# Kernel optimization log

Hardware: AMD Instinct MI355X
Metric: run time of the kernel (lower is better)

Reference implementation:

```python
import jax, jax.numpy as jnp
import numpy as np

N = 50000       # nodes
E = 1600000     # edges (avg degree 32)
IN = 128        # node_in_dim
D = 64          # node_out_dim (= GRU hidden)
H = 1           # heads
ED = 3          # edge_in_dim
STEPS = 3       # num_step_message_passing
EPS = 1e-5      # BatchNorm eps
SLOPE = 0.2     # LeakyReLU negative slope (GAT default)


def setup_inputs() -> dict:
    key = jax.random.key(0)
    ks = jax.random.split(key, 16)
    s_in = 1.0 / np.sqrt(IN)
    s_d = 1.0 / np.sqrt(D)
    return {
        "x": jax.random.normal(ks[0], (N, IN), jnp.float32),
        "edge_attr": jax.random.normal(ks[1], (E, ED), jnp.float32),
        "mlp_w": jax.random.normal(ks[2], (IN, D), jnp.float32) * s_in,
        "mlp_b": jnp.zeros((D,), jnp.float32),
        "bn_g": jnp.ones((D,), jnp.float32),
        "bn_b": jnp.zeros((D,), jnp.float32),
        "conv_w": jax.random.normal(ks[3], (D, H * D), jnp.float32) * s_d,
        "att_dst": jax.random.normal(ks[4], (H, D), jnp.float32) * s_d,
        "att_src": jax.random.normal(ks[5], (H, D), jnp.float32) * s_d,
        "att_edge": jax.random.normal(ks[6], (H, ED), jnp.float32) * s_d,
        "w_ih": jax.random.normal(ks[7], (3 * D, H * D), jnp.float32) * s_d,
        "w_hh": jax.random.normal(ks[8], (3 * D, D), jnp.float32) * s_d,
        "b_ih": jnp.zeros((3 * D,), jnp.float32),
        "b_hh": jnp.zeros((3 * D,), jnp.float32),
        "lin_w": jax.random.normal(ks[9], (IN, D), jnp.float32) * s_in,
        "lin_b": jnp.zeros((D,), jnp.float32),
        "edge_index": jax.random.randint(ks[10], (2, E), 0, N, jnp.int64),
    }


def _egat_conv(out, edge_attr, src, dst, conv_w, att_dst, att_src, att_edge):
    # out: [N, D] -> xt: [N, H, D]
    xt = (out @ conv_w).reshape(N, H, D)
    # per-node attention halves (avoid gathering twice): [N, H]
    a_dst_n = jnp.einsum("nhd,hd->nh", xt, att_dst)
    a_src_n = jnp.einsum("nhd,hd->nh", xt, att_src)
    # per-edge logits: [E, H]
    logits = a_dst_n[dst] + a_src_n[src] + edge_attr @ att_edge.T
    logits = jnp.where(logits >= 0, logits, SLOPE * logits)
    # segment softmax over destination nodes
    seg_max = jax.ops.segment_max(logits, dst, num_segments=N)  # [N, H]
    seg_max = jnp.where(jnp.isfinite(seg_max), seg_max, 0.0)
    expd = jnp.exp(logits - seg_max[dst])
    denom = jax.ops.segment_sum(expd, dst, num_segments=N)      # [N, H]
    alpha = expd / denom[dst]                                   # [E, H]
    # attention-weighted aggregation of source features
    msgs = alpha[:, :, None] * xt[src]                          # [E, H, D]
    agg = jax.ops.segment_sum(msgs, dst, num_segments=N)        # [N, H, D]
    return agg.reshape(N, H * D)


def _gru_cell(x_in, h, w_ih, w_hh, b_ih, b_hh):
    gi = x_in @ w_ih.T + b_ih
    gh = h @ w_hh.T + b_hh
    gi_r, gi_z, gi_n = jnp.split(gi, 3, axis=-1)
    gh_r, gh_z, gh_n = jnp.split(gh, 3, axis=-1)
    r = jax.nn.sigmoid(gi_r + gh_r)
    z = jax.nn.sigmoid(gi_z + gh_z)
    n = jnp.tanh(gi_n + r * gh_n)
    return (1.0 - z) * n + z * h


def reference(x, edge_attr, mlp_w, mlp_b, bn_g, bn_b, conv_w, att_dst,
              att_src, att_edge, w_ih, w_hh, b_ih, b_hh, lin_w, lin_b,
              edge_index):
    src, dst = edge_index[0], edge_index[1]
    # initial embedding: ReLU(BatchNorm(Linear(x))) with batch stats
    h0 = x @ mlp_w + mlp_b
    mu = jnp.mean(h0, axis=0)
    var = jnp.var(h0, axis=0)
    out = jax.nn.relu((h0 - mu) * jax.lax.rsqrt(var + EPS) * bn_g + bn_b)
    h = out
    for _ in range(STEPS):
        m = jax.nn.relu(_egat_conv(out, edge_attr, src, dst,
                                   conv_w, att_dst, att_src, att_edge))
        h = _gru_cell(m, h, w_ih, w_hh, b_ih, b_hh)
        out = h
    return x @ lin_w + lin_b + out
```

## Files before the change

kernel.cpp:

```cpp
#include <hip/hip_runtime.h>

typedef unsigned short ushort_t;
typedef unsigned int uint_t;
typedef __attribute__((ext_vector_type(8))) short bf16x8;
typedef __attribute__((ext_vector_type(4))) float f32x4;

#define N_NODES 50000
#define N_EDGES 1600000
#define NB_BKT 391
#define CAP_BKT 4608
#define CAP_B 6144
#define GBK 782
#define WPAD 72
#define APAD 64

__device__ __forceinline__ float bfu(ushort_t u) {
    return __uint_as_float(((uint_t)u) << 16);
}
__device__ __forceinline__ ushort_t f2b(float f) {
    uint_t x = __float_as_uint(f);
    uint_t r = (x + 0x7FFFu + ((x >> 16) & 1u)) >> 16;
    return (ushort_t)r;
}
__device__ __forceinline__ float sigm(float x) {
    return 1.0f / (1.0f + __expf(-x));
}
__device__ __forceinline__ float tanh_f(float x) {
    return 1.0f - 2.0f / (__expf(2.0f * x) + 1.0f);
}
__device__ __forceinline__ bf16x8 pack8(const float* v) {
    bf16x8 r;
#pragma unroll
    for (int j = 0; j < 8; ++j) r[j] = (short)f2b(v[j]);
    return r;
}
__device__ __forceinline__ int ld_src(const int* __restrict__ ei, int i, int f64) {
    return f64 ? ei[2 * i] : ei[i];
}
__device__ __forceinline__ int ld_dst(const int* __restrict__ ei, int i, int f64) {
    return f64 ? ei[2 * N_EDGES + 2 * i] : ei[N_EDGES + i];
}
__device__ __forceinline__ bool is_f64(const int* flag) { return flag[0] > 2048; }

__global__ void k_sentinel(float* __restrict__ out, int n) {
    int i = blockIdx.x * 256 + threadIdx.x;
    if (i < n) out[i] = 100.0f;
}

__global__ void k_prep(const float* __restrict__ w_ih, const float* __restrict__ w_hh,
                       const float* __restrict__ conv_w, const float* __restrict__ mlp_w,
                       const float* __restrict__ lin_w, const int* __restrict__ ei,
                       ushort_t* __restrict__ wb, ushort_t* __restrict__ cwb,
                       ushort_t* __restrict__ mlpT, ushort_t* __restrict__ linT,
                       int* __restrict__ flag, int* __restrict__ gtail) {
    int blk = blockIdx.x;
    if (blk < 176) {
        int t = blk * 256 + threadIdx.x;
        if (t < 24576) {
            const float* w = (t < 12288) ? w_ih : w_hh;
            wb[t] = f2b(w[t < 12288 ? t : t - 12288]);
        } else if (t < 28672) {
            int r = t - 24576;
            int j = r >> 6, k = r & 63;
            cwb[j * 64 + k] = f2b(conv_w[k * 64 + j]);
        } else if (t < 36864) {
            int r = t - 28672;
            int j = r >> 7, k = r & 127;
            mlpT[j * 128 + k] = f2b(mlp_w[k * 64 + j]);
        } else if (t < 45056) {
            int r = t - 36864;
            int j = r >> 7, k = r & 127;
            linT[j * 128 + k] = f2b(lin_w[k * 64 + j]);
        }
    } else if (blk == 176) {
        __shared__ int red[256];
        int tid = threadIdx.x;
        int zeros = 0;
#pragma unroll
        for (int j = 0; j < 16; ++j) {
            int slot = (tid * 16 + j) * 2 + 1;
            if (ei[slot] == 0) zeros++;
        }
        red[tid] = zeros;
        __syncthreads();
        for (int off = 128; off; off >>= 1) {
            if (tid < off) red[tid] += red[tid + off];
            __syncthreads();
        }
        if (tid == 0) flag[0] = red[0];
    } else {
        int b = (blk - 177) * 256 + threadIdx.x;
        if (b < NB_BKT) gtail[b * APAD] = b * CAP_BKT;
    }
}

__global__ __launch_bounds__(256) void k_embbkt(
    const int* __restrict__ ei, const int* __restrict__ flag,
    const float* __restrict__ ea, const float* __restrict__ ae,
    int* __restrict__ gtail, uint2* __restrict__ bkt, int e,
    const float* __restrict__ x, const ushort_t* __restrict__ mlpT,
    const float* __restrict__ mlp_b, float* __restrict__ h0, int n) {
    if (blockIdx.x < GBK) {
        __shared__ int cnt[NB_BKT];
        __shared__ int gbase[NB_BKT];
        for (int i = threadIdx.x; i < NB_BKT; i += 256) cnt[i] = 0;
        __syncthreads();
        int base = blockIdx.x * 2048;
        int f64 = is_f64(flag);
        float a0 = ae[0], a1 = ae[1], a2 = ae[2];
        uint_t w0[8], w1[8];
        int bk[8], rk[8];
#pragma unroll
        for (int j = 0; j < 8; ++j) {
            int i = base + j * 256 + threadIdx.x;
            bk[j] = -1;
            if (i < e) {
                int d = ld_dst(ei, i, f64);
                if ((uint_t)d < (uint_t)N_NODES) {
                    int s = ld_src(ei, i, f64);
                    if ((uint_t)s >= (uint_t)N_NODES) s = 0;
                    float ed = ea[i * 3] * a0 + ea[i * 3 + 1] * a1 + ea[i * 3 + 2] * a2;
                    bk[j] = d >> 7;
                    w0[j] = (uint_t)s | ((uint_t)(d & 127) << 16);
                    w1[j] = __float_as_uint(ed);
                    rk[j] = atomicAdd(&cnt[bk[j]], 1);
                }
            }
        }
        __syncthreads();
        for (int t = threadIdx.x; t < NB_BKT; t += 256) {
            int c = cnt[t];
            gbase[t] = c ? atomicAdd(&gtail[t * APAD], c) : 0;
        }
        __syncthreads();
#pragma unroll
        for (int j = 0; j < 8; ++j) {
            if (bk[j] >= 0) {
                int pos = gbase[bk[j]] + rk[j];
                if (pos < (bk[j] + 1) * CAP_BKT) {
                    uint2 p;
                    p.x = w0[j];
                    p.y = w1[j];
                    bkt[pos] = p;
                }
            }
        }
    } else {
        int lane = threadIdx.x & 63;
        int wv = threadIdx.x >> 6;
        int tile = (blockIdx.x - GBK) * 4 + wv;
        if (tile * 16 >= n) return;
        int nb16 = tile * 16;
        int mrow = lane & 15, q = lane >> 4;
        const float* xp = x + (nb16 + mrow) * 128 + q * 8;
        bf16x8 a[4];
#pragma unroll
        for (int kc = 0; kc < 4; ++kc) {
            float hv[8];
            const float* p = xp + kc * 32;
#pragma unroll
            for (int j = 0; j < 8; ++j) hv[j] = p[j];
            a[kc] = pack8(hv);
        }
        f32x4 acc[4];
#pragma unroll
        for (int t = 0; t < 4; ++t) acc[t] = (f32x4){0.f, 0.f, 0.f, 0.f};
#pragma unroll
        for (int kc = 0; kc < 4; ++kc) {
#pragma unroll
            for (int t = 0; t < 4; ++t) {
                bf16x8 b =
                    *(const bf16x8*)(mlpT + (t * 16 + mrow) * 128 + kc * 32 + q * 8);
                acc[t] = __builtin_amdgcn_mfma_f32_16x16x32_bf16(a[kc], b, acc[t], 0, 0, 0);
            }
        }
#pragma unroll
        for (int t = 0; t < 4; ++t) {
            int j = t * 16 + mrow;
            float bias = mlp_b[j];
#pragma unroll
            for (int r = 0; r < 4; ++r)
                h0[(nb16 + q * 4 + r) * 64 + j] = acc[t][r] + bias;
        }
    }
}

__global__ __launch_bounds__(256) void k_statsort(
    const int* __restrict__ gtail, const uint2* __restrict__ bkt,
    uint_t* __restrict__ pk, int* __restrict__ rs, int n,
    const float* __restrict__ h0, float* __restrict__ stats) {
    __shared__ char smem[26624];
    int tid = threadIdx.x;
    if (blockIdx.x < NB_BKT) {
        int* red = (int*)smem;
        int* cnt = (int*)(smem + 1024);
        int* sc = (int*)(smem + 1536);
        uint_t* stg = (uint_t*)(smem + 2048);
        int b = blockIdx.x;
        int partial = 0;
        for (int i = tid; i < b; i += 256)
            partial += min(gtail[i * APAD] - i * CAP_BKT, CAP_BKT);
        red[tid] = partial;
        __syncthreads();
        for (int off = 128; off; off >>= 1) {
            if (tid < off) red[tid] += red[tid + off];
            __syncthreads();
        }
        int obase = red[0];
        int node0 = b * 128;
        int nloc = min(128, n - node0);
        int size = min(gtail[b * APAD] - b * CAP_BKT, CAP_BKT);
        const uint2* bin = bkt + b * CAP_BKT;
        for (int i = tid; i < 128; i += 256) cnt[i] = 0;
        __syncthreads();
        for (int ofs = tid; ofs < size; ofs += 256) {
            int dlow = (bin[ofs].x >> 16) & 127;
            atomicAdd(&cnt[dlow], 1);
        }
        __syncthreads();
        if (tid < 128) sc[tid] = cnt[tid];
        __syncthreads();
        for (int off = 1; off < 128; off <<= 1) {
            int add = (tid < 128 && tid >= off) ? sc[tid - off] : 0;
            __syncthreads();
            if (tid < 128) sc[tid] += add;
            __syncthreads();
        }
        if (tid < 128) sc[tid] -= cnt[tid];
        __syncthreads();
        if (tid < nloc) rs[node0 + tid] = obase + sc[tid];
        if (b == NB_BKT - 1 && tid == 0) rs[n] = obase + size;
        for (int i = tid; i < 128; i += 256) cnt[i] = 0;
        __syncthreads();
        for (int ofs = tid; ofs < size; ofs += 256) {
            uint2 p = bin[ofs];
            int dlow = (p.x >> 16) & 127;
            int r = atomicAdd(&cnt[dlow], 1);
            int pos = sc[dlow] + r;
            uint_t q = (p.x & 0xFFFFu) | ((uint_t)f2b(__uint_as_float(p.y)) << 16);
            if (pos < CAP_B) stg[pos] = q;
            else pk[obase + pos] = q;
        }
        __syncthreads();
        int wlim = min(size, CAP_B);
        for (int ofs = tid; ofs < wlim; ofs += 256) pk[obase + ofs] = stg[ofs];
    } else {
        float* ssum = (float*)smem;
        float* ssq = (float*)(smem + 1024);
        int gid = (blockIdx.x - NB_BKT) * 256 + tid;
        int col = gid & 63;
        int rg = gid >> 6;
        float s = 0.f, s2 = 0.f;
        for (int row = rg; row < n; row += 1024) {
            float v = h0[row * 64 + col];
            s += v;
            s2 += v * v;
        }
        ssum[tid] = s;
        ssq[tid] = s2;
        __syncthreads();
        if (tid < 64) {
            s = ssum[tid] + ssum[tid + 64] + ssum[tid + 128] + ssum[tid + 192];
            s2 = ssq[tid] + ssq[tid + 64] + ssq[tid + 128] + ssq[tid + 192];
            atomicAdd(&stats[tid * APAD], s);
            atomicAdd(&stats[(64 + tid) * APAD], s2);
        }
    }
}

__global__ __launch_bounds__(256) void k_xt(float* __restrict__ h,
                                            const ushort_t* __restrict__ cwb,
                                            const float* __restrict__ att_dst,
                                            const float* __restrict__ att_src,
                                            const float* __restrict__ bn_g,
                                            const float* __restrict__ bn_b,
                                            const float* __restrict__ stats,
                                            float inv_n,
                                            ushort_t* __restrict__ xt,
                                            float* __restrict__ adst,
                                            float* __restrict__ asrc, int n) {
    __shared__ float scb[64], shb[64];
    {
        int tid = threadIdx.x;
        if (tid < 64) {
            float mu = stats[tid * APAD] * inv_n;
            float var = fmaxf(stats[(64 + tid) * APAD] * inv_n - mu * mu, 0.f);
            float sc = rsqrtf(var + 1e-5f) * bn_g[tid];
            scb[tid] = sc;
            shb[tid] = bn_b[tid] - mu * sc;
        }
        __syncthreads();
    }
    int lane = threadIdx.x & 63;
    int wv = threadIdx.x >> 6;
    int tile = blockIdx.x * 4 + wv;
    if (tile * 16 >= n) return;
    int nb16 = tile * 16;
    int mrow = lane & 15, q = lane >> 4;
    bf16x8 ah[2];
    {
        float* hp = h + (nb16 + mrow) * 64 + q * 8;
        float hv[8];
#pragma unroll
        for (int kh = 0; kh < 2; ++kh) {
            float* p = hp + kh * 32;
            int cb = kh * 32 + q * 8;
#pragma unroll
            for (int j = 0; j < 8; ++j) {
                hv[j] = fmaxf(p[j] * scb[cb + j] + shb[cb + j], 0.f);
                p[j] = hv[j];
            }
            ah[kh] = pack8(hv);
        }
    }
    f32x4 acc[4];
#pragma unroll
    for (int t = 0; t < 4; ++t) acc[t] = (f32x4){0.f, 0.f, 0.f, 0.f};
#pragma unroll
    for (int kh = 0; kh < 2; ++kh) {
#pragma unroll
        for (int t = 0; t < 4; ++t) {
            bf16x8 b = *(const bf16x8*)(cwb + (t * 16 + mrow) * 64 + kh * 32 + q * 8);
            acc[t] = __builtin_amdgcn_mfma_f32_16x16x32_bf16(ah[kh], b, acc[t], 0, 0, 0);
        }
    }
    float sd[4] = {0, 0, 0, 0}, ss[4] = {0, 0, 0, 0};
#pragma unroll
    for (int t = 0; t < 4; ++t) {
        int j = t * 16 + mrow;
        float ad = att_dst[j], as = att_src[j];
#pragma unroll
        for (int r = 0; r < 4; ++r) {
            float v = acc[t][r];
            xt[(nb16 + q * 4 + r) * 64 + j] = f2b(v);
            sd[r] += v * ad;
            ss[r] += v * as;
        }
    }
#pragma unroll
    for (int off = 1; off < 16; off <<= 1) {
#pragma unroll
        for (int r = 0; r < 4; ++r) {
            sd[r] += __shfl_xor(sd[r], off);
            ss[r] += __shfl_xor(ss[r], off);
        }
    }
    if (mrow == 0) {
#pragma unroll
        for (int r = 0; r < 4; ++r) {
            adst[nb16 + q * 4 + r] = sd[r];
            asrc[nb16 + q * 4 + r] = ss[r];
        }
    }
}

__global__ __launch_bounds__(256) void k_agg(const int* __restrict__ rs,
                                             const uint_t* __restrict__ pk,
                                             const float* __restrict__ adst,
                                             const float* __restrict__ asrc,
                                             const ushort_t* __restrict__ xt,
                                             ushort_t* __restrict__ m, int n) {
    __shared__ float s_w[4][64];
    __shared__ int s_s[4][64];
    int lane = threadIdx.x & 63;
    int wv = threadIdx.x >> 6;
    int v = blockIdx.x * 4 + wv;
    if (v >= n) return;
    int start = rs[v], end = rs[v + 1];
    if (start >= end) {
        m[v * 64 + lane] = 0;
        return;
    }
    float adv = adst[v];
    int g = lane >> 3;
    int cb = (lane & 7) * 8;
    float acc[8] = {0, 0, 0, 0, 0, 0, 0, 0};
    float dsum = 0.f;
    for (int base = start; base < end; base += 64) {
        int e = base + lane;
        float w = 0.f;
        int s = 0;
        if (e < end) {
            uint_t p = pk[e];
            s = (int)(p & 0xFFFFu);
            float l = adv + asrc[s] + bfu((ushort_t)(p >> 16));
            l = (l >= 0.f) ? l : 0.2f * l;
            w = __expf(l);
        }
        dsum += w;
        s_w[wv][lane] = w;
        s_s[wv][lane] = s;
        int cnt = min(64, end - base);
        int nb8 = (cnt + 7) >> 3;
        for (int tb = 0; tb < nb8; ++tb) {
            int sl = tb * 8 + g;
            float w8 = s_w[wv][sl];
            int s8 = s_s[wv][sl];
            uint4 qv = *(const uint4*)(xt + s8 * 64 + cb);
            acc[0] += w8 * __uint_as_float(qv.x << 16);
            acc[1] += w8 * __uint_as_float(qv.x & 0xFFFF0000u);
            acc[2] += w8 * __uint_as_float(qv.y << 16);
            acc[3] += w8 * __uint_as_float(qv.y & 0xFFFF0000u);
            acc[4] += w8 * __uint_as_float(qv.z << 16);
            acc[5] += w8 * __uint_as_float(qv.z & 0xFFFF0000u);
            acc[6] += w8 * __uint_as_float(qv.w << 16);
            acc[7] += w8 * __uint_as_float(qv.w & 0xFFFF0000u);
        }
    }
#pragma unroll
    for (int off = 32; off; off >>= 1) dsum += __shfl_xor(dsum, off);
#pragma unroll
    for (int off = 8; off < 64; off <<= 1) {
#pragma unroll
        for (int j = 0; j < 8; ++j) acc[j] += __shfl_xor(acc[j], off);
    }
    float inv = 1.0f / fmaxf(dsum, 1e-20f);
    if (g == 0) {
        uint4 o;
        o.x = (uint_t)f2b(fmaxf(acc[0] * inv, 0.f)) |
              ((uint_t)f2b(fmaxf(acc[1] * inv, 0.f)) << 16);
        o.y = (uint_t)f2b(fmaxf(acc[2] * inv, 0.f)) |
              ((uint_t)f2b(fmaxf(acc[3] * inv, 0.f)) << 16);
        o.z = (uint_t)f2b(fmaxf(acc[4] * inv, 0.f)) |
              ((uint_t)f2b(fmaxf(acc[5] * inv, 0.f)) << 16);
        o.w = (uint_t)f2b(fmaxf(acc[6] * inv, 0.f)) |
              ((uint_t)f2b(fmaxf(acc[7] * inv, 0.f)) << 16);
        *(uint4*)(m + v * 64 + cb) = o;
    }
}

__global__ __launch_bounds__(256) void k_gruxt(
    const ushort_t* __restrict__ mb, float* __restrict__ h,
    const ushort_t* __restrict__ wb, const ushort_t* __restrict__ cwb,
    const float* __restrict__ b_ih, const float* __restrict__ b_hh,
    const float* __restrict__ att_dst, const float* __restrict__ att_src,
    int do_xt, ushort_t* __restrict__ xt, float* __restrict__ adst,
    float* __restrict__ asrc, int n) {
    __shared__ ushort_t swb[384 * WPAD];
    __shared__ ushort_t scw[64 * WPAD];
    {
        const uint2* src = (const uint2*)wb;
        for (int g = threadIdx.x; g < 6144; g += 256) {
            uint2 v = src[g];
            int row = g >> 4;
            int col = (g & 15) * 4;
            *(uint2*)(swb + row * WPAD + col) = v;
        }
        const uint2* srcc = (const uint2*)cwb;
        for (int g = threadIdx.x; g < 1024; g += 256) {
            uint2 v = srcc[g];
            int row = g >> 4;
            int col = (g & 15) * 4;
            *(uint2*)(scw + row * WPAD + col) = v;
        }
    }
    __syncthreads();
    int lane = threadIdx.x & 63;
    int wv = threadIdx.x >> 6;
    int tile = blockIdx.x * 4 + wv;
    if (tile * 16 >= n) return;
    int nb16 = tile * 16;
    int mrow = lane & 15, q = lane >> 4;
    float hp[4][4];
#pragma unroll
    for (int t = 0; t < 4; ++t)
#pragma unroll
        for (int r = 0; r < 4; ++r)
            hp[t][r] = h[(nb16 + q * 4 + r) * 64 + t * 16 + mrow];
    bf16x8 am[2], ah[2];
    {
        const ushort_t* mp = mb + (nb16 + mrow) * 64 + q * 8;
        am[0] = *(const bf16x8*)(mp);
        am[1] = *(const bf16x8*)(mp + 32);
        const float* hpt = h + (nb16 + mrow) * 64 + q * 8;
        float hv[8];
#pragma unroll
        for (int j = 0; j < 8; ++j) hv[j] = hpt[j];
        ah[0] = pack8(hv);
#pragma unroll
        for (int j = 0; j < 8; ++j) hv[j] = hpt[32 + j];
        ah[1] = pack8(hv);
    }
    f32x4 acc[24];
#pragma unroll
    for (int t = 0; t < 24; ++t) acc[t] = (f32x4){0.f, 0.f, 0.f, 0.f};
#pragma unroll
    for (int kh = 0; kh < 2; ++kh) {
#pragma unroll
        for (int t = 0; t < 12; ++t) {
            bf16x8 b = *(const bf16x8*)(swb + (t * 16 + mrow) * WPAD + kh * 32 + q * 8);
            acc[t] = __builtin_amdgcn_mfma_f32_16x16x32_bf16(am[kh], b, acc[t], 0, 0, 0);
        }
#pragma unroll
        for (int t = 0; t < 12; ++t) {
            bf16x8 b =
                *(const bf16x8*)(swb + (192 + t * 16 + mrow) * WPAD + kh * 32 + q * 8);
            acc[12 + t] =
                __builtin_amdgcn_mfma_f32_16x16x32_bf16(ah[kh], b, acc[12 + t], 0, 0, 0);
        }
    }
#pragma unroll
    for (int t = 0; t < 4; ++t) {
        int j = t * 16 + mrow;
        float bir = b_ih[j], biz = b_ih[64 + j], bin = b_ih[128 + j];
        float bhr = b_hh[j], bhz = b_hh[64 + j], bhn = b_hh[128 + j];
#pragma unroll
        for (int r = 0; r < 4; ++r) {
            int node = nb16 + q * 4 + r;
            float gr = acc[t][r] + bir + acc[12 + t][r] + bhr;
            float gz = acc[4 + t][r] + biz + acc[16 + t][r] + bhz;
            float rr = sigm(gr);
            float zz = sigm(gz);
            float tt = acc[8 + t][r] + bin + rr * (acc[20 + t][r] + bhn);
            h[node * 64 + j] = (1.f - zz) * tanh_f(tt) + zz * hp[t][r];
        }
    }
    if (!do_xt) return;
    __threadfence_block();
    bf16x8 ah2[2];
    {
        const float* hpt = h + (nb16 + mrow) * 64 + q * 8;
        float hv[8];
#pragma unroll
        for (int j = 0; j < 8; ++j) hv[j] = hpt[j];
        ah2[0] = pack8(hv);
#pragma unroll
        for (int j = 0; j < 8; ++j) hv[j] = hpt[32 + j];
        ah2[1] = pack8(hv);
    }
    f32x4 xacc[4];
#pragma unroll
    for (int t = 0; t < 4; ++t) xacc[t] = (f32x4){0.f, 0.f, 0.f, 0.f};
#pragma unroll
    for (int kh = 0; kh < 2; ++kh) {
#pragma unroll
        for (int t = 0; t < 4; ++t) {
            bf16x8 b = *(const bf16x8*)(scw + (t * 16 + mrow) * WPAD + kh * 32 + q * 8);
            xacc[t] = __builtin_amdgcn_mfma_f32_16x16x32_bf16(ah2[kh], b, xacc[t], 0, 0, 0);
        }
    }
    float sd[4] = {0, 0, 0, 0}, ss[4] = {0, 0, 0, 0};
#pragma unroll
    for (int t = 0; t < 4; ++t) {
        int j = t * 16 + mrow;
        float ad = att_dst[j], as = att_src[j];
#pragma unroll
        for (int r = 0; r < 4; ++r) {
            float v = xacc[t][r];
            xt[(nb16 + q * 4 + r) * 64 + j] = f2b(v);
            sd[r] += v * ad;
            ss[r] += v * as;
        }
    }
#pragma unroll
    for (int off = 1; off < 16; off <<= 1) {
#pragma unroll
        for (int r = 0; r < 4; ++r) {
            sd[r] += __shfl_xor(sd[r], off);
            ss[r] += __shfl_xor(ss[r], off);
        }
    }
    if (mrow == 0) {
#pragma unroll
        for (int r = 0; r < 4; ++r) {
            adst[nb16 + q * 4 + r] = sd[r];
            asrc[nb16 + q * 4 + r] = ss[r];
        }
    }
}

__global__ __launch_bounds__(256) void k_out(const float* __restrict__ x,
                                             const ushort_t* __restrict__ linT,
                                             const float* __restrict__ lin_b,
                                             const float* __restrict__ h,
                                             float* __restrict__ out, int n) {
    int lane = threadIdx.x & 63;
    int wv = threadIdx.x >> 6;
    int tile = blockIdx.x * 4 + wv;
    if (tile * 16 >= n) return;
    int nb16 = tile * 16;
    int mrow = lane & 15, q = lane >> 4;
    const float* xp = x + (nb16 + mrow) * 128 + q * 8;
    bf16x8 a[4];
#pragma unroll
    for (int kc = 0; kc < 4; ++kc) {
        float hv[8];
        const float* p = xp + kc * 32;
#pragma unroll
        for (int j = 0; j < 8; ++j) hv[j] = p[j];
        a[kc] = pack8(hv);
    }
    f32x4 acc[4];
#pragma unroll
    for (int t = 0; t < 4; ++t) acc[t] = (f32x4){0.f, 0.f, 0.f, 0.f};
#pragma unroll
    for (int kc = 0; kc < 4; ++kc) {
#pragma unroll
        for (int t = 0; t < 4; ++t) {
            bf16x8 b = *(const bf16x8*)(linT + (t * 16 + mrow) * 128 + kc * 32 + q * 8);
            acc[t] = __builtin_amdgcn_mfma_f32_16x16x32_bf16(a[kc], b, acc[t], 0, 0, 0);
        }
    }
#pragma unroll
    for (int t = 0; t < 4; ++t) {
        int j = t * 16 + mrow;
        float bias = lin_b[j];
#pragma unroll
        for (int r = 0; r < 4; ++r) {
            int node = nb16 + q * 4 + r;
            out[node * 64 + j] = acc[t][r] + bias + h[node * 64 + j];
        }
    }
}

extern "C" void kernel_launch(void* const* d_in, const int* in_sizes, int n_in,
                              void* d_out, int out_size, void* d_ws, size_t ws_size,
                              hipStream_t stream) {
    const float* x = (const float*)d_in[0];
    const float* edge_attr = (const float*)d_in[1];
    const float* mlp_w = (const float*)d_in[2];
    const float* mlp_b = (const float*)d_in[3];
    const float* bn_g = (const float*)d_in[4];
    const float* bn_b = (const float*)d_in[5];
    const float* conv_w = (const float*)d_in[6];
    const float* att_dst = (const float*)d_in[7];
    const float* att_src = (const float*)d_in[8];
    const float* att_edge = (const float*)d_in[9];
    const float* w_ih = (const float*)d_in[10];
    const float* w_hh = (const float*)d_in[11];
    const float* b_ih = (const float*)d_in[12];
    const float* b_hh = (const float*)d_in[13];
    const float* lin_w = (const float*)d_in[14];
    const float* lin_b = (const float*)d_in[15];
    const int* ei = (const int*)d_in[16];

    char* ws = (char*)d_ws;
    float* f_h = (float*)(ws + 0);
    ushort_t* mb = (ushort_t*)(ws + 12800000);
    ushort_t* xt = (ushort_t*)(ws + 19200000);
    uint2* bkt = (uint2*)(ws + 25600000);
    uint_t* pk = (uint_t*)(ws + 40013824);
    float* f_adst = (float*)(ws + 46413824);
    float* f_asrc = (float*)(ws + 46614016);
    int* row_start = (int*)(ws + 46814208);
    float* stats = (float*)(ws + 47014656);
    int* flag = (int*)(ws + 47047424);
    ushort_t* wb = (ushort_t*)(ws + 47047936);
    ushort_t* cwb = (ushort_t*)(ws + 47097088);
    ushort_t* mlpT = (ushort_t*)(ws + 47105280);
    ushort_t* linT = (ushort_t*)(ws + 47121664);
    int* gtail = (int*)(ws + 47138048);

    const size_t needed = 47238144;
    if (ws_size < needed) {
        k_sentinel<<<(out_size + 255) / 256, 256, 0, stream>>>((float*)d_out, out_size);
        return;
    }

    const int n = N_NODES, e = N_EDGES;
    const int gT = ((n + 15) / 16 + 3) / 4;
    const int gN4 = (n + 3) / 4;
    const int gPrep = 176 + 1 + (NB_BKT + 255) / 256;
    const float inv_n = 1.0f / (float)n;

    hipMemsetAsync(stats, 0, 32768, stream);

    k_prep<<<gPrep, 256, 0, stream>>>(w_ih, w_hh, conv_w, mlp_w, lin_w, ei, wb, cwb,
                                      mlpT, linT, flag, gtail);
    k_embbkt<<<GBK + gT, 256, 0, stream>>>(ei, flag, edge_attr, att_edge, gtail, bkt, e,
                                           x, mlpT, mlp_b, f_h, n);
    k_statsort<<<NB_BKT + 256, 256, 0, stream>>>(gtail, bkt, pk, row_start, n, f_h,
                                                 stats);
    k_xt<<<gT, 256, 0, stream>>>(f_h, cwb, att_dst, att_src, bn_g, bn_b, stats, inv_n,
                                 xt, f_adst, f_asrc, n);

    for (int s = 0; s < 3; ++s) {
        k_agg<<<gN4, 256, 0, stream>>>(row_start, pk, f_adst, f_asrc, xt, mb, n);
        k_gruxt<<<gT, 256, 0, stream>>>(mb, f_h, wb, cwb, b_ih, b_hh, att_dst, att_src,
                                        (s < 2) ? 1 : 0, xt, f_adst, f_asrc, n);
    }

    k_out<<<gT, 256, 0, stream>>>(x, linT, lin_b, f_h, (float*)d_out, n);
}
```

Before: 368.8 us.

## Compute source attention logits from gathered features in aggregation; enlarge bucketing blocks

The aggregation kernel stops doing a separate random gather of the per-node source attention scalar. Instead it computes the source logit by dotting the already-gathered bf16 xt row with att_src, reduced across 8 lanes with shuffles, and then applies LeakyReLU and exp per edge inside the inner loop. This removes one scattered load per edge but adds extra FMAs, shuffles and exps per 8-edge group, and the logit now comes from bf16 xt rather than the fp32 asrc. Separately, the edge-bucketing kernel now processes 4096 edges per block with half as many blocks, so fewer global atomics are issued on the bucket tails.

```diff
diff --git a/kernel.cpp b/kernel.cpp
--- a/kernel.cpp
+++ b/kernel.cpp
@@ -10,7 +10,7 @@
 #define NB_BKT 391
 #define CAP_BKT 4608
 #define CAP_B 6144
-#define GBK 782
+#define GBK 391
 #define WPAD 72
 #define APAD 64
 
@@ -105,13 +105,13 @@
         __shared__ int gbase[NB_BKT];
         for (int i = threadIdx.x; i < NB_BKT; i += 256) cnt[i] = 0;
         __syncthreads();
-        int base = blockIdx.x * 2048;
+        int base = blockIdx.x * 4096;
         int f64 = is_f64(flag);
         float a0 = ae[0], a1 = ae[1], a2 = ae[2];
-        uint_t w0[8], w1[8];
-        int bk[8], rk[8];
-#pragma unroll
-        for (int j = 0; j < 8; ++j) {
+        uint_t w0[16], w1[16];
+        int bk[16], rk[16];
+#pragma unroll
+        for (int j = 0; j < 16; ++j) {
             int i = base + j * 256 + threadIdx.x;
             bk[j] = -1;
             if (i < e) {
@@ -134,7 +134,7 @@
         }
         __syncthreads();
 #pragma unroll
-        for (int j = 0; j < 8; ++j) {
+        for (int j = 0; j < 16; ++j) {
             if (bk[j] >= 0) {
                 int pos = gbase[bk[j]] + rk[j];
                 if (pos < (bk[j] + 1) * CAP_BKT) {
@@ -357,7 +357,7 @@
 __global__ __launch_bounds__(256) void k_agg(const int* __restrict__ rs,
                                              const uint_t* __restrict__ pk,
                                              const float* __restrict__ adst,
-                                             const float* __restrict__ asrc,
+                                             const float* __restrict__ att_src,
                                              const ushort_t* __restrict__ xt,
                                              ushort_t* __restrict__ m, int n) {
     __shared__ float s_w[4][64];
@@ -374,41 +374,59 @@
     float adv = adst[v];
     int g = lane >> 3;
     int cb = (lane & 7) * 8;
+    float asv[8];
+#pragma unroll
+    for (int j = 0; j < 8; ++j) asv[j] = att_src[cb + j];
     float acc[8] = {0, 0, 0, 0, 0, 0, 0, 0};
     float dsum = 0.f;
     for (int base = start; base < end; base += 64) {
         int e = base + lane;
-        float w = 0.f;
+        float et = 0.f;
         int s = 0;
         if (e < end) {
             uint_t p = pk[e];
             s = (int)(p & 0xFFFFu);
-            float l = adv + asrc[s] + bfu((ushort_t)(p >> 16));
-            l = (l >= 0.f) ? l : 0.2f * l;
-            w = __expf(l);
-        }
-        dsum += w;
-        s_w[wv][lane] = w;
+            et = bfu((ushort_t)(p >> 16));
+        }
+        s_w[wv][lane] = et;
         s_s[wv][lane] = s;
         int cnt = min(64, end - base);
         int nb8 = (cnt + 7) >> 3;
         for (int tb = 0; tb < nb8; ++tb) {
             int sl = tb * 8 + g;
-            float w8 = s_w[wv][sl];
+            float et8 = s_w[wv][sl];
             int s8 = s_s[wv][sl];
             uint4 qv = *(const uint4*)(xt + s8 * 64 + cb);
-            acc[0] += w8 * __uint_as_float(qv.x << 16);
-            acc[1] += w8 * __uint_as_float(qv.x & 0xFFFF0000u);
-            acc[2] += w8 * __uint_as_float(qv.y << 16);
-            acc[3] += w8 * __uint_as_float(qv.y & 0xFFFF0000u);
-            acc[4] += w8 * __uint_as_float(qv.z << 16);
-            acc[5] += w8 * __uint_as_float(qv.z & 0xFFFF0000u);
-            acc[6] += w8 * __uint_as_float(qv.w << 16);
-            acc[7] += w8 * __uint_as_float(qv.w & 0xFFFF0000u);
-        }
-    }
-#pragma unroll
-    for (int off = 32; off; off >>= 1) dsum += __shfl_xor(dsum, off);
+            float f0 = __uint_as_float(qv.x << 16);
+            float f1 = __uint_as_float(qv.x & 0xFFFF0000u);
+            float f2 = __uint_as_float(qv.y << 16);
+            float f3 = __uint_as_float(qv.y & 0xFFFF0000u);
+            float f4 = __uint_as_float(qv.z << 16);
+            float f5 = __uint_as_float(qv.z & 0xFFFF0000u);
+            float f6 = __uint_as_float(qv.w << 16);
+            float f7 = __uint_as_float(qv.w & 0xFFFF0000u);
+            float part = f0 * asv[0] + f1 * asv[1] + f2 * asv[2] + f3 * asv[3] +
+                         f4 * asv[4] + f5 * asv[5] + f6 * asv[6] + f7 * asv[7];
+            part += __shfl_xor(part, 1);
+            part += __shfl_xor(part, 2);
+            part += __shfl_xor(part, 4);
+            float l = adv + part + et8;
+            l = (l >= 0.f) ? l : 0.2f * l;
+            float w8 = (sl < cnt) ? __expf(l) : 0.f;
+            dsum += w8;
+            acc[0] += w8 * f0;
+            acc[1] += w8 * f1;
+            acc[2] += w8 * f2;
+            acc[3] += w8 * f3;
+            acc[4] += w8 * f4;
+            acc[5] += w8 * f5;
+            acc[6] += w8 * f6;
+            acc[7] += w8 * f7;
+        }
+    }
+    dsum += __shfl_xor(dsum, 8);
+    dsum += __shfl_xor(dsum, 16);
+    dsum += __shfl_xor(dsum, 32);
 #pragma unroll
     for (int off = 8; off < 64; off <<= 1) {
 #pragma unroll
@@ -675,7 +693,7 @@
                                  xt, f_adst, f_asrc, n);
 
     for (int s = 0; s < 3; ++s) {
-        k_agg<<<gN4, 256, 0, stream>>>(row_start, pk, f_adst, f_asrc, xt, mb, n);
+        k_agg<<<gN4, 256, 0, stream>>>(row_start, pk, f_adst, att_src, xt, mb, n);
         k_gruxt<<<gT, 256, 0, stream>>>(mb, f_h, wb, cwb, b_ih, b_hh, att_dst, att_src,
                                         (s < 2) ? 1 : 0, xt, f_adst, f_asrc, n);
     }
```

New measurement: 384.7 us. 1.04x slower.
